# Optimization experiments

Hardware: AMD Instinct MI355X
Metric: run time of the kernel (lower is better)

The kernel has to match this reference:

```python
import jax, jax.numpy as jnp
import numpy as np

IN_FEATS, H_FEATS, OUT_FEATS = 128, 256, 64
N_NODES, N_EDGES = 50000, 800000
DROP_P = 0.5


def setup_inputs() -> dict:
    key = jax.random.key(0)
    k_h, k_e, k_w1, k_w2 = jax.random.split(key, 4)
    h = jax.random.normal(k_h, (N_NODES, IN_FEATS), dtype=jnp.float32)
    edge_index = jax.random.randint(k_e, (2, N_EDGES), 0, N_NODES, dtype=jnp.int64)
    # Glorot-style init for GraphConv weights; bias zeros (DGL default)
    W1 = jax.random.normal(k_w1, (IN_FEATS, H_FEATS), dtype=jnp.float32) / np.sqrt(IN_FEATS)
    b1 = jnp.zeros((H_FEATS,), dtype=jnp.float32)
    W2 = jax.random.normal(k_w2, (H_FEATS, OUT_FEATS), dtype=jnp.float32) / np.sqrt(H_FEATS)
    b2 = jnp.zeros((OUT_FEATS,), dtype=jnp.float32)
    return {"h": h, "W1": W1, "b1": b1, "W2": W2, "b2": b2,
            "edge_index": edge_index, "n_nodes": N_NODES}


def _sym_norm(edge_index, n_nodes):
    # symmetric GCN norm: deg^-1/2 on both endpoints (in-degree, clamped to 1)
    dst = edge_index[1]
    deg = jax.ops.segment_sum(jnp.ones(edge_index.shape[1], jnp.float32), dst,
                              num_segments=n_nodes)
    return jnp.where(deg > 0, deg, 1.0) ** -0.5  # [N]


def _graph_conv(h, W, b, src, dst, norm, n_nodes, apply_w_first):
    # DGL GraphConv (norm='both'): scale by src norm, aggregate, scale by dst norm.
    # W is applied before aggregation if in_feats > out_feats, else after.
    x = h * norm[:, None]
    if apply_w_first:
        x = x @ W
    agg = jax.ops.segment_sum(x[src], dst, num_segments=n_nodes)
    if not apply_w_first:
        agg = agg @ W
    return agg * norm[:, None] + b


def reference(h, W1, b1, W2, b2, edge_index, n_nodes):
    src, dst = edge_index[0], edge_index[1]
    norm = _sym_norm(edge_index, n_nodes)
    # layer 1: in(128) <= out(256) -> aggregate then transform; relu activation
    h1 = jax.nn.relu(_graph_conv(h, W1, b1, src, dst, norm, n_nodes, apply_w_first=False))
    # dropout(0.5), training mode, deterministic key
    keep = jax.random.bernoulli(jax.random.key(42), 1.0 - DROP_P, h1.shape)
    h1 = jnp.where(keep, h1 / (1.0 - DROP_P), 0.0)
    # layer 2: in(256) > out(64) -> transform then aggregate; no activation
    out = _graph_conv(h1, W2, b2, src, dst, norm, n_nodes, apply_w_first=True)
    return out
```

## Files before the change

kernel.cpp:

```cpp
#include <hip/hip_runtime.h>
#include <stdint.h>

#define N_IN  128
#define N_H   256
#define N_OUT 64
#define CHK   2048
#define CAP   6144

typedef __attribute__((ext_vector_type(8))) __bf16 bf16x8;
typedef __attribute__((ext_vector_type(4))) float f32x4;

__device__ __forceinline__ void tf4(uint32_t& x0, uint32_t& x1,
                                    const int r0, const int r1, const int r2, const int r3) {
  x0 += x1; x1 = (x1 << r0) | (x1 >> (32 - r0)); x1 ^= x0;
  x0 += x1; x1 = (x1 << r1) | (x1 >> (32 - r1)); x1 ^= x0;
  x0 += x1; x1 = (x1 << r2) | (x1 >> (32 - r2)); x1 ^= x0;
  x0 += x1; x1 = (x1 << r3) | (x1 >> (32 - r3)); x1 ^= x0;
}

__device__ __forceinline__ uint2 threefry2x32(uint32_t k0, uint32_t k1, uint32_t x0, uint32_t x1) {
  const uint32_t k2 = k0 ^ k1 ^ 0x1BD11BDAu;
  x0 += k0; x1 += k1;
  tf4(x0, x1, 13, 15, 26, 6);   x0 += k1; x1 += k2 + 1u;
  tf4(x0, x1, 17, 29, 16, 24);  x0 += k2; x1 += k0 + 2u;
  tf4(x0, x1, 13, 15, 26, 6);   x0 += k0; x1 += k1 + 3u;
  tf4(x0, x1, 17, 29, 16, 24);  x0 += k1; x1 += k2 + 4u;
  tf4(x0, x1, 13, 15, 26, 6);   x0 += k2; x1 += k0 + 5u;
  return make_uint2(x0, x1);
}

__device__ __forceinline__ uint16_t f2bf_rne(float v) {
  uint32_t b = __builtin_bit_cast(uint32_t, v);
  b += 0x7fffu + ((b >> 16) & 1u);
  return (uint16_t)(b >> 16);
}
__device__ __forceinline__ float bflo(uint32_t w) { return __builtin_bit_cast(float, w << 16); }
__device__ __forceinline__ float bfhi(uint32_t w) { return __builtin_bit_cast(float, w & 0xffff0000u); }

__device__ __forceinline__ void packW_body(const float* __restrict__ W,
                                           uint4* __restrict__ WH, uint4* __restrict__ WL,
                                           int Ncols, int nct, int nks, int g) {
  if (g >= nct * nks * 64) return;
  int lane = g & 63;
  int grp = g >> 6;
  int ks = grp % nks, ct = grp / nks;
  int k0 = ks * 32 + (lane >> 4) * 8;
  int col = ct * 16 + (lane & 15);
  uint32_t hb[8], lb[8];
#pragma unroll
  for (int j = 0; j < 8; j++) {
    float w = W[(size_t)(k0 + j) * Ncols + col];
    uint32_t bits = __builtin_bit_cast(uint32_t, w);
    uint32_t hi = bits & 0xffff0000u;
    float lo = w - __builtin_bit_cast(float, hi);
    hb[j] = hi >> 16;
    lb[j] = __builtin_bit_cast(uint32_t, lo) >> 16;
  }
  WH[g] = make_uint4(hb[0] | (hb[1] << 16), hb[2] | (hb[3] << 16),
                     hb[4] | (hb[5] << 16), hb[6] | (hb[7] << 16));
  WL[g] = make_uint4(lb[0] | (lb[1] << 16), lb[2] | (lb[3] << 16),
                     lb[4] | (lb[5] << 16), lb[6] | (lb[7] << 16));
}

__global__ __launch_bounds__(256) void k_front(
    const int* __restrict__ eidx, int E, int* __restrict__ bktCur, uint2* __restrict__ eb,
    uint16_t* __restrict__ mask, int N,
    const float* __restrict__ W1, uint4* __restrict__ W1H, uint4* __restrict__ W1L,
    const float* __restrict__ W2, uint4* __restrict__ W2H, uint4* __restrict__ W2L,
    int NBE) {
  const int b = blockIdx.x, t = threadIdx.x;
  if (b < NBE) {
    __shared__ int s_nz;
    __shared__ int hist[256];
    __shared__ int base[256];
    if (t == 0) s_nz = 0;
    hist[t] = 0;
    __syncthreads();
    int n = E < 2048 ? E : 2048;
    int nz = 0;
    for (int i = t; i < n; i += 256) nz |= (eidx[2 * i + 1] != 0) ? 1 : 0;
    if (nz) atomicAdd(&s_nz, 1);
    __syncthreads();
    int stride = (s_nz == 0) ? 2 : 1;

    int cb = b * CHK;
    int dc[8], sc[8];
#pragma unroll
    for (int i = 0; i < 8; i++) {
      int e = cb + i * 256 + t;
      if (e < E) {
        dc[i] = eidx[(size_t)(E + e) * stride];
        sc[i] = eidx[(size_t)e * stride];
        atomicAdd(&hist[dc[i] >> 8], 1);
      } else dc[i] = -1;
    }
    __syncthreads();
    int hcnt = hist[t];
    if (hcnt) base[t] = atomicAdd(&bktCur[t], hcnt);
    __syncthreads();
    hist[t] = 0;
    __syncthreads();
#pragma unroll
    for (int i = 0; i < 8; i++) {
      if (dc[i] >= 0) {
        int bk = dc[i] >> 8;
        int r = atomicAdd(&hist[bk], 1);
        eb[(size_t)bk * CAP + base[bk] + r] = make_uint2((unsigned)sc[i], (unsigned)dc[i]);
      }
    }
  } else {
    const int NBM = (N * 16 + 255) >> 8;
    int bb = b - NBE;
    if (bb < NBM) {
      int g = bb * 256 + t;
      if (g >= N * 16) return;
      uint32_t row = (uint32_t)(g >> 4), colb = (uint32_t)(g & 15);
      uint32_t bse = row * 256u + colb;
      uint32_t m = 0;
#pragma unroll
      for (int ct = 0; ct < 16; ct++) {
        uint2 o = threefry2x32(0u, 42u, 0u, bse + (uint32_t)ct * 16u);
        uint32_t bits = o.x ^ o.y;
        m |= ((~bits) >> 31) << ct;
      }
      mask[g] = (uint16_t)m;
    } else if (bb < NBM + 16) {
      packW_body(W1, W1H, W1L, N_H, 16, 4, (bb - NBM) * 256 + t);
    } else {
      packW_body(W2, W2H, W2L, N_OUT, 4, 8, (bb - NBM - 16) * 256 + t);
    }
  }
}

__global__ __launch_bounds__(256) void k_bucket_csr(
    const uint2* __restrict__ eb, const int* __restrict__ bktCur,
    int* __restrict__ rowptr, float* __restrict__ norm,
    int* __restrict__ esrc, int N, int E) {
  __shared__ int s[256];
  __shared__ int cnt[256];
  __shared__ int pfx[256];
  __shared__ int cur[256];
  const int b = blockIdx.x, t = threadIdx.x;
  if (b == 0 && t == 0) rowptr[N] = E;
  if (b * 256 >= N) return;
  int xc = bktCur[t];
  s[t] = xc;
  __syncthreads();
  for (int off = 1; off < 256; off <<= 1) {
    int u = (t >= off) ? s[t - off] : 0;
    __syncthreads();
    s[t] += u;
    __syncthreads();
  }
  const int lo = (b > 0) ? s[b - 1] : 0;
  const int ecnt = s[b] - lo;
  const uint2* ebb = eb + (size_t)b * CAP;
  cnt[t] = 0;
  __syncthreads();
  for (int e = t; e < ecnt; e += 256)
    atomicAdd(&cnt[ebb[e].y & 255u], 1);
  __syncthreads();
  int x = cnt[t];
  pfx[t] = x;
  __syncthreads();
  for (int off = 1; off < 256; off <<= 1) {
    int u = (t >= off) ? pfx[t - off] : 0;
    __syncthreads();
    pfx[t] += u;
    __syncthreads();
  }
  int excl = pfx[t] - x;
  int node = b * 256 + t;
  if (node < N) {
    rowptr[node] = lo + excl;
    norm[node] = x > 0 ? rsqrtf((float)x) : 1.0f;
  }
  cur[t] = excl;
  __syncthreads();
  for (int e = t; e < ecnt; e += 256) {
    uint2 r = ebb[e];
    int d = (int)(r.y & 255u);
    int p = atomicAdd(&cur[d], 1);
    esrc[lo + p] = (int)r.x;
  }
}

__global__ __launch_bounds__(256) void k_mid(
    int* __restrict__ esrc, const int* __restrict__ rowptr, int N,
    const float* __restrict__ h, const float* __restrict__ norm,
    uint16_t* __restrict__ hn, int NS) {
  const int b = blockIdx.x, t = threadIdx.x;
  if (b < NS) {
    int node = b * 4 + (t >> 6);
    if (node >= N) return;
    const int lane = t & 63;
    int lo = rowptr[node], hi = rowptr[node + 1], d = hi - lo;
    if (d <= 1) return;
    if (d <= 64) {
      int v = (lane < d) ? esrc[lo + lane] : 0x7fffffff;
#pragma unroll
      for (int k = 2; k <= 64; k <<= 1) {
#pragma unroll
        for (int j = k >> 1; j > 0; j >>= 1) {
          int other = __shfl_xor(v, j);
          bool up = ((lane & k) == 0);
          bool lower = ((lane & j) == 0);
          int mn = min(v, other), mx = max(v, other);
          v = (up == lower) ? mn : mx;
        }
      }
      if (lane < d) esrc[lo + lane] = v;
    } else if (lane == 0) {
      for (int i = lo + 1; i < hi; i++) {
        int v = esrc[i];
        int j = i - 1;
        while (j >= lo && esrc[j] > v) { esrc[j + 1] = esrc[j]; j--; }
        esrc[j + 1] = v;
      }
    }
  } else {
    int g = (b - NS) * 256 + t;
    if (g >= N * 32) return;
    float nr = norm[g >> 5];
    float4 v = *reinterpret_cast<const float4*>(h + (size_t)g * 4);
    ushort4 r;
    r.x = f2bf_rne(v.x * nr);
    r.y = f2bf_rne(v.y * nr);
    r.z = f2bf_rne(v.z * nr);
    r.w = f2bf_rne(v.w * nr);
    *reinterpret_cast<ushort4*>(hn + (size_t)g * 4) = r;
  }
}

__global__ __launch_bounds__(256) void k_pull1(
    const uint16_t* __restrict__ hn, const int* __restrict__ rowptr,
    const int* __restrict__ esrc, uint16_t* __restrict__ aggB, int N) {
  int node = blockIdx.x * 8 + (threadIdx.x >> 5);
  if (node >= N) return;
  int lane = threadIdx.x & 31;
  int lo = rowptr[node], hi = rowptr[node + 1];
  float4 a0 = {0,0,0,0}, a1 = {0,0,0,0}, a2 = {0,0,0,0}, a3 = {0,0,0,0};
  int e = lo;
  for (; e + 7 < hi; e += 8) {
    int s0 = esrc[e],     s1 = esrc[e + 1], s2 = esrc[e + 2], s3 = esrc[e + 3];
    int s4 = esrc[e + 4], s5 = esrc[e + 5], s6 = esrc[e + 6], s7 = esrc[e + 7];
    uint2 v0 = *reinterpret_cast<const uint2*>(hn + (size_t)s0 * N_IN + lane * 4);
    uint2 v1 = *reinterpret_cast<const uint2*>(hn + (size_t)s1 * N_IN + lane * 4);
    uint2 v2 = *reinterpret_cast<const uint2*>(hn + (size_t)s2 * N_IN + lane * 4);
    uint2 v3 = *reinterpret_cast<const uint2*>(hn + (size_t)s3 * N_IN + lane * 4);
    uint2 v4 = *reinterpret_cast<const uint2*>(hn + (size_t)s4 * N_IN + lane * 4);
    uint2 v5 = *reinterpret_cast<const uint2*>(hn + (size_t)s5 * N_IN + lane * 4);
    uint2 v6 = *reinterpret_cast<const uint2*>(hn + (size_t)s6 * N_IN + lane * 4);
    uint2 v7 = *reinterpret_cast<const uint2*>(hn + (size_t)s7 * N_IN + lane * 4);
    a0.x += bflo(v0.x); a0.y += bfhi(v0.x); a0.z += bflo(v0.y); a0.w += bfhi(v0.y);
    a1.x += bflo(v1.x); a1.y += bfhi(v1.x); a1.z += bflo(v1.y); a1.w += bfhi(v1.y);
    a2.x += bflo(v2.x); a2.y += bfhi(v2.x); a2.z += bflo(v2.y); a2.w += bfhi(v2.y);
    a3.x += bflo(v3.x); a3.y += bfhi(v3.x); a3.z += bflo(v3.y); a3.w += bfhi(v3.y);
    a0.x += bflo(v4.x); a0.y += bfhi(v4.x); a0.z += bflo(v4.y); a0.w += bfhi(v4.y);
    a1.x += bflo(v5.x); a1.y += bfhi(v5.x); a1.z += bflo(v5.y); a1.w += bfhi(v5.y);
    a2.x += bflo(v6.x); a2.y += bfhi(v6.x); a2.z += bflo(v6.y); a2.w += bfhi(v6.y);
    a3.x += bflo(v7.x); a3.y += bfhi(v7.x); a3.z += bflo(v7.y); a3.w += bfhi(v7.y);
  }
  for (; e < hi; e++) {
    uint2 v0 = *reinterpret_cast<const uint2*>(hn + (size_t)esrc[e] * N_IN + lane * 4);
    a0.x += bflo(v0.x); a0.y += bfhi(v0.x); a0.z += bflo(v0.y); a0.w += bfhi(v0.y);
  }
  float4 r;
  r.x = (a0.x + a1.x) + (a2.x + a3.x);
  r.y = (a0.y + a1.y) + (a2.y + a3.y);
  r.z = (a0.z + a1.z) + (a2.z + a3.z);
  r.w = (a0.w + a1.w) + (a2.w + a3.w);
  ushort4 p = make_ushort4(f2bf_rne(r.x), f2bf_rne(r.y), f2bf_rne(r.z), f2bf_rne(r.w));
  *reinterpret_cast<ushort4*>(aggB + (size_t)node * N_IN + lane * 4) = p;
}

__global__ __launch_bounds__(256) void k_gemm12(
    const uint16_t* __restrict__ aggB,
    const uint4* __restrict__ W1H, const uint4* __restrict__ W1L,
    const float* __restrict__ b1, const float* __restrict__ norm,
    const uint16_t* __restrict__ mask,
    const uint4* __restrict__ W2H, const uint4* __restrict__ W2L,
    uint16_t* __restrict__ zbf, int Nn) {
  __shared__ uint16_t h1[64 * 256];
  __shared__ uint4 wlds[2048];
  const int tid = threadIdx.x;
  const int wave = tid >> 6, lane = tid & 63;
  const int row0 = blockIdx.x * 64 + wave * 16;
  const int lrow = lane & 15, lk = lane >> 4;
  int arow = row0 + lrow; if (arow >= Nn) arow = Nn - 1;

  uint4 aq[4];
#pragma unroll
  for (int ks = 0; ks < 4; ks++)
    aq[ks] = *reinterpret_cast<const uint4*>(aggB + (size_t)arow * N_IN + ks * 32 + lk * 8);

  f32x4 acc[16];
#pragma unroll
  for (int c = 0; c < 16; c++) acc[c] = f32x4{0.f, 0.f, 0.f, 0.f};

  for (int ks = 0; ks < 4; ks++) {
    __syncthreads();
#pragma unroll
    for (int i = 0; i < 4; i++) {
      int g = tid + i * 256;
      int src = ((g >> 6) * 4 + ks) * 64 + (g & 63);
      wlds[g]        = W1H[src];
      wlds[1024 + g] = W1L[src];
    }
    __syncthreads();
    union { uint4 q; bf16x8 v; } ah; ah.q = aq[ks];
#pragma unroll
    for (int c = 0; c < 16; c++) {
      union { uint4 q; bf16x8 v; } bh, bl;
      bh.q = wlds[c * 64 + lane];
      bl.q = wlds[1024 + c * 64 + lane];
      acc[c] = __builtin_amdgcn_mfma_f32_16x16x32_bf16(ah.v, bh.v, acc[c], 0, 0, 0);
      acc[c] = __builtin_amdgcn_mfma_f32_16x16x32_bf16(ah.v, bl.v, acc[c], 0, 0, 0);
    }
  }

  const int colb = lane & 15, rgrp = lane >> 4;
#pragma unroll
  for (int r = 0; r < 4; r++) {
    int lrw = wave * 16 + rgrp * 4 + r;
    int row = blockIdx.x * 64 + lrw;
    float nr = (row < Nn) ? norm[row] : 0.f;
    uint32_t m = (row < Nn) ? (uint32_t)mask[row * 16 + colb] : 0u;
    int sw = (lrw & 7) << 3;
#pragma unroll
    for (int c = 0; c < 16; c++) {
      int col = c * 16 + colb;
      float v = fmaf(acc[c][r], nr, b1[col]);
      v = fmaxf(v, 0.f);
      v = ((m >> c) & 1u) ? v * (2.0f * nr) : 0.f;
      h1[lrw * 256 + (col ^ sw)] = f2bf_rne(v);
    }
  }

  f32x4 acc2[4];
#pragma unroll
  for (int c = 0; c < 4; c++) acc2[c] = f32x4{0.f, 0.f, 0.f, 0.f};
  const int myrow = wave * 16 + lrow;
  const int sw2 = (myrow & 7) << 3;

  for (int half = 0; half < 2; half++) {
    __syncthreads();
#pragma unroll
    for (int i = 0; i < 4; i++) {
      int g = tid + i * 256;
      int src = ((g >> 8) * 8 + half * 4 + ((g >> 6) & 3)) * 64 + (g & 63);
      wlds[g]        = W2H[src];
      wlds[1024 + g] = W2L[src];
    }
    __syncthreads();
#pragma unroll
    for (int ksl = 0; ksl < 4; ksl++) {
      int ks = half * 4 + ksl;
      union { uint4 q; bf16x8 v; } ah;
      int c0 = (ks * 32 + lk * 8) ^ sw2;
      ah.q = *reinterpret_cast<const uint4*>(&h1[myrow * 256 + c0]);
#pragma unroll
      for (int c = 0; c < 4; c++) {
        union { uint4 q; bf16x8 v; } bh, bl;
        bh.q = wlds[(c * 4 + ksl) * 64 + lane];
        bl.q = wlds[1024 + (c * 4 + ksl) * 64 + lane];
        acc2[c] = __builtin_amdgcn_mfma_f32_16x16x32_bf16(ah.v, bh.v, acc2[c], 0, 0, 0);
        acc2[c] = __builtin_amdgcn_mfma_f32_16x16x32_bf16(ah.v, bl.v, acc2[c], 0, 0, 0);
      }
    }
  }
#pragma unroll
  for (int r = 0; r < 4; r++) {
    int row = row0 + rgrp * 4 + r;
    if (row >= Nn) continue;
#pragma unroll
    for (int c = 0; c < 4; c++)
      zbf[(size_t)row * N_OUT + c * 16 + colb] = f2bf_rne(acc2[c][r]);
  }
}

__global__ __launch_bounds__(256) void k_pull2(
    const uint16_t* __restrict__ zbf, const float* __restrict__ norm,
    const float* __restrict__ b2, const int* __restrict__ rowptr,
    const int* __restrict__ esrc, float* __restrict__ out, int N) {
  int node = blockIdx.x * 16 + (threadIdx.x >> 4);
  if (node >= N) return;
  int lane = threadIdx.x & 15;
  int lo = rowptr[node], hi = rowptr[node + 1];
  float4 a0 = {0,0,0,0}, a1 = {0,0,0,0}, a2 = {0,0,0,0}, a3 = {0,0,0,0};
  int e = lo;
  for (; e + 7 < hi; e += 8) {
    int s0 = esrc[e],     s1 = esrc[e + 1], s2 = esrc[e + 2], s3 = esrc[e + 3];
    int s4 = esrc[e + 4], s5 = esrc[e + 5], s6 = esrc[e + 6], s7 = esrc[e + 7];
    uint2 v0 = *reinterpret_cast<const uint2*>(zbf + (size_t)s0 * N_OUT + lane * 4);
    uint2 v1 = *reinterpret_cast<const uint2*>(zbf + (size_t)s1 * N_OUT + lane * 4);
    uint2 v2 = *reinterpret_cast<const uint2*>(zbf + (size_t)s2 * N_OUT + lane * 4);
    uint2 v3 = *reinterpret_cast<const uint2*>(zbf + (size_t)s3 * N_OUT + lane * 4);
    uint2 v4 = *reinterpret_cast<const uint2*>(zbf + (size_t)s4 * N_OUT + lane * 4);
    uint2 v5 = *reinterpret_cast<const uint2*>(zbf + (size_t)s5 * N_OUT + lane * 4);
    uint2 v6 = *reinterpret_cast<const uint2*>(zbf + (size_t)s6 * N_OUT + lane * 4);
    uint2 v7 = *reinterpret_cast<const uint2*>(zbf + (size_t)s7 * N_OUT + lane * 4);
    a0.x += bflo(v0.x); a0.y += bfhi(v0.x); a0.z += bflo(v0.y); a0.w += bfhi(v0.y);
    a1.x += bflo(v1.x); a1.y += bfhi(v1.x); a1.z += bflo(v1.y); a1.w += bfhi(v1.y);
    a2.x += bflo(v2.x); a2.y += bfhi(v2.x); a2.z += bflo(v2.y); a2.w += bfhi(v2.y);
    a3.x += bflo(v3.x); a3.y += bfhi(v3.x); a3.z += bflo(v3.y); a3.w += bfhi(v3.y);
    a0.x += bflo(v4.x); a0.y += bfhi(v4.x); a0.z += bflo(v4.y); a0.w += bfhi(v4.y);
    a1.x += bflo(v5.x); a1.y += bfhi(v5.x); a1.z += bflo(v5.y); a1.w += bfhi(v5.y);
    a2.x += bflo(v6.x); a2.y += bfhi(v6.x); a2.z += bflo(v6.y); a2.w += bfhi(v6.y);
    a3.x += bflo(v7.x); a3.y += bfhi(v7.x); a3.z += bflo(v7.y); a3.w += bfhi(v7.y);
  }
  for (; e < hi; e++) {
    uint2 v0 = *reinterpret_cast<const uint2*>(zbf + (size_t)esrc[e] * N_OUT + lane * 4);
    a0.x += bflo(v0.x); a0.y += bfhi(v0.x); a0.z += bflo(v0.y); a0.w += bfhi(v0.y);
  }
  float nn = norm[node];
  float4 bb = *reinterpret_cast<const float4*>(b2 + lane * 4);
  float4 r;
  r.x = ((a0.x + a1.x) + (a2.x + a3.x)) * nn + bb.x;
  r.y = ((a0.y + a1.y) + (a2.y + a3.y)) * nn + bb.y;
  r.z = ((a0.z + a1.z) + (a2.z + a3.z)) * nn + bb.z;
  r.w = ((a0.w + a1.w) + (a2.w + a3.w)) * nn + bb.w;
  *reinterpret_cast<float4*>(out + (size_t)node * N_OUT + lane * 4) = r;
}

extern "C" void kernel_launch(void* const* d_in, const int* in_sizes, int n_in,
                              void* d_out, int out_size, void* d_ws, size_t ws_size,
                              hipStream_t stream) {
  const float* h  = (const float*)d_in[0];
  const float* W1 = (const float*)d_in[1];
  const float* b1 = (const float*)d_in[2];
  const float* W2 = (const float*)d_in[3];
  const float* b2 = (const float*)d_in[4];
  const int* eidx = (const int*)d_in[5];
  const int N = in_sizes[0] / N_IN;
  const int E = in_sizes[5] / 2;
  const int NBE = (E + CHK - 1) / CHK;
  const int NBM = (N * 16 + 255) / 256;
  const int NS  = (N + 3) / 4;
  const int NH  = (N * 32 + 255) / 256;

  char* ws = (char*)d_ws;
  size_t off = 0;
  auto alloc = [&](size_t bytes) { void* p = ws + off; off += (bytes + 511) & ~(size_t)511; return p; };
  int*      rowptr = (int*)alloc((size_t)(N + 1) * 4);
  float*    norm   = (float*)alloc((size_t)N * 4);
  int*      esrc   = (int*)alloc((size_t)E * 4);
  int*      bktCur = (int*)alloc((size_t)256 * 4);
  uint16_t* mask   = (uint16_t*)alloc((size_t)N * 16 * 2);
  uint4*    W1H    = (uint4*)alloc((size_t)16 * 4 * 64 * 16);
  uint4*    W1L    = (uint4*)alloc((size_t)16 * 4 * 64 * 16);
  uint4*    W2H    = (uint4*)alloc((size_t)4 * 8 * 64 * 16);
  uint4*    W2L    = (uint4*)alloc((size_t)4 * 8 * 64 * 16);
  uint2*    eb     = (uint2*)alloc((size_t)256 * CAP * 8);
  uint16_t* hn     = (uint16_t*)alloc((size_t)N * N_IN * 2);
  uint16_t* aggB   = (uint16_t*)alloc((size_t)N * N_IN * 2);
  uint16_t* zbf    = (uint16_t*)alloc((size_t)N * N_OUT * 2);
  float*    out    = (float*)d_out;

  hipMemsetAsync(bktCur, 0, 256 * 4, stream);

  k_front<<<NBE + NBM + 16 + 8, 256, 0, stream>>>(eidx, E, bktCur, eb,
                                                  mask, N, W1, W1H, W1L, W2, W2H, W2L, NBE);

  k_bucket_csr<<<256, 256, 0, stream>>>(eb, bktCur, rowptr, norm, esrc, N, E);

  k_mid<<<NS + NH, 256, 0, stream>>>(esrc, rowptr, N, h, norm, hn, NS);

  k_pull1<<<(N + 7) / 8, 256, 0, stream>>>(hn, rowptr, esrc, aggB, N);

  k_gemm12<<<(N + 63) / 64, 256, 0, stream>>>(aggB, W1H, W1L, b1, norm, mask,
                                              W2H, W2L, zbf, N);

  k_pull2<<<(N + 15) / 16, 256, 0, stream>>>(zbf, norm, b2, rowptr, esrc, out, N);
}
```

Measured before the change: 145.9 us.

## Fuse hn conversion into CSR build and sort neighbor lists inside pull kernels

After: 153.1 us. 5.0% more time.

```diff
diff --git a/kernel.cpp b/kernel.cpp
--- a/kernel.cpp
+++ b/kernel.cpp
@@ -36,6 +36,22 @@
 }
 __device__ __forceinline__ float bflo(uint32_t w) { return __builtin_bit_cast(float, w << 16); }
 __device__ __forceinline__ float bfhi(uint32_t w) { return __builtin_bit_cast(float, w & 0xffff0000u); }
+__device__ __forceinline__ float bfu16(uint16_t w) { return __builtin_bit_cast(float, (uint32_t)w << 16); }
+
+__device__ __forceinline__ int bitonic64(int v, int lane) {
+#pragma unroll
+  for (int k = 2; k <= 64; k <<= 1) {
+#pragma unroll
+    for (int j = k >> 1; j > 0; j >>= 1) {
+      int other = __shfl_xor(v, j);
+      bool up = ((lane & k) == 0);
+      bool lower = ((lane & j) == 0);
+      int mn = min(v, other), mx = max(v, other);
+      v = (up == lower) ? mn : mx;
+    }
+  }
+  return v;
+}
 
 __device__ __forceinline__ void packW_body(const float* __restrict__ W,
                                            uint4* __restrict__ WH, uint4* __restrict__ WL,
@@ -135,11 +151,13 @@
 __global__ __launch_bounds__(256) void k_bucket_csr(
     const uint2* __restrict__ eb, const int* __restrict__ bktCur,
     int* __restrict__ rowptr, float* __restrict__ norm,
-    int* __restrict__ esrc, int N, int E) {
+    int* __restrict__ esrc, const float* __restrict__ h,
+    uint16_t* __restrict__ hn, int N, int E) {
   __shared__ int s[256];
   __shared__ int cnt[256];
   __shared__ int pfx[256];
   __shared__ int cur[256];
+  __shared__ float narr[256];
   const int b = blockIdx.x, t = threadIdx.x;
   if (b == 0 && t == 0) rowptr[N] = E;
   if (b * 256 >= N) return;
@@ -171,9 +189,11 @@
   }
   int excl = pfx[t] - x;
   int node = b * 256 + t;
+  float nrm = x > 0 ? rsqrtf((float)x) : 1.0f;
+  narr[t] = nrm;
   if (node < N) {
     rowptr[node] = lo + excl;
-    norm[node] = x > 0 ? rsqrtf((float)x) : 1.0f;
+    norm[node] = nrm;
   }
   cur[t] = excl;
   __syncthreads();
@@ -183,34 +203,66 @@
     int p = atomicAdd(&cur[d], 1);
     esrc[lo + p] = (int)r.x;
   }
-}
-
-__global__ __launch_bounds__(256) void k_mid(
-    int* __restrict__ esrc, const int* __restrict__ rowptr, int N,
-    const float* __restrict__ h, const float* __restrict__ norm,
-    uint16_t* __restrict__ hn, int NS) {
-  const int b = blockIdx.x, t = threadIdx.x;
-  if (b < NS) {
-    int node = b * 4 + (t >> 6);
-    if (node >= N) return;
-    const int lane = t & 63;
-    int lo = rowptr[node], hi = rowptr[node + 1], d = hi - lo;
-    if (d <= 1) return;
-    if (d <= 64) {
-      int v = (lane < d) ? esrc[lo + lane] : 0x7fffffff;
-#pragma unroll
-      for (int k = 2; k <= 64; k <<= 1) {
-#pragma unroll
-        for (int j = k >> 1; j > 0; j >>= 1) {
-          int other = __shfl_xor(v, j);
-          bool up = ((lane & k) == 0);
-          bool lower = ((lane & j) == 0);
-          int mn = min(v, other), mx = max(v, other);
-          v = (up == lower) ? mn : mx;
-        }
-      }
-      if (lane < d) esrc[lo + lane] = v;
-    } else if (lane == 0) {
+  const int nrows = min(256, N - b * 256);
+#pragma unroll 4
+  for (int i = 0; i < 32; i++) {
+    int g = i * 256 + t;
+    int r = g >> 5;
+    if (r >= nrows) break;
+    int c4 = g & 31;
+    size_t row = (size_t)(b * 256 + r);
+    float4 v = *reinterpret_cast<const float4*>(h + row * N_IN + c4 * 4);
+    float nr = narr[r];
+    ushort4 o;
+    o.x = f2bf_rne(v.x * nr);
+    o.y = f2bf_rne(v.y * nr);
+    o.z = f2bf_rne(v.z * nr);
+    o.w = f2bf_rne(v.w * nr);
+    *reinterpret_cast<ushort4*>(hn + row * N_IN + c4 * 4) = o;
+  }
+}
+
+__global__ __launch_bounds__(256) void k_pull1s(
+    const uint16_t* __restrict__ hn, const int* __restrict__ rowptr,
+    int* esrc, uint16_t* __restrict__ aggB, int N) {
+  int node = blockIdx.x * 4 + (threadIdx.x >> 6);
+  if (node >= N) return;
+  const int lane = threadIdx.x & 63;
+  int lo = rowptr[node], hi = rowptr[node + 1], d = hi - lo;
+  float2 a0 = {0,0}, a1 = {0,0}, a2 = {0,0}, a3 = {0,0};
+  if (d <= 64) {
+    int v = (lane < d) ? esrc[lo + lane] : 0x7fffffff;
+    if (d > 1) v = bitonic64(v, lane);
+    int e = 0;
+    for (; e + 7 < d; e += 8) {
+      int s0 = __shfl(v, e),     s1 = __shfl(v, e + 1);
+      int s2 = __shfl(v, e + 2), s3 = __shfl(v, e + 3);
+      int s4 = __shfl(v, e + 4), s5 = __shfl(v, e + 5);
+      int s6 = __shfl(v, e + 6), s7 = __shfl(v, e + 7);
+      uint32_t u0 = *reinterpret_cast<const uint32_t*>(hn + (size_t)s0 * N_IN + lane * 2);
+      uint32_t u1 = *reinterpret_cast<const uint32_t*>(hn + (size_t)s1 * N_IN + lane * 2);
+      uint32_t u2 = *reinterpret_cast<const uint32_t*>(hn + (size_t)s2 * N_IN + lane * 2);
+      uint32_t u3 = *reinterpret_cast<const uint32_t*>(hn + (size_t)s3 * N_IN + lane * 2);
+      uint32_t u4 = *reinterpret_cast<const uint32_t*>(hn + (size_t)s4 * N_IN + lane * 2);
+      uint32_t u5 = *reinterpret_cast<const uint32_t*>(hn + (size_t)s5 * N_IN + lane * 2);
+      uint32_t u6 = *reinterpret_cast<const uint32_t*>(hn + (size_t)s6 * N_IN + lane * 2);
+      uint32_t u7 = *reinterpret_cast<const uint32_t*>(hn + (size_t)s7 * N_IN + lane * 2);
+      a0.x += bflo(u0); a0.y += bfhi(u0);
+      a1.x += bflo(u1); a1.y += bfhi(u1);
+      a2.x += bflo(u2); a2.y += bfhi(u2);
+      a3.x += bflo(u3); a3.y += bfhi(u3);
+      a0.x += bflo(u4); a0.y += bfhi(u4);
+      a1.x += bflo(u5); a1.y += bfhi(u5);
+      a2.x += bflo(u6); a2.y += bfhi(u6);
+      a3.x += bflo(u7); a3.y += bfhi(u7);
+    }
+    for (; e < d; e++) {
+      int s0 = __shfl(v, e);
+      uint32_t u0 = *reinterpret_cast<const uint32_t*>(hn + (size_t)s0 * N_IN + lane * 2);
+      a0.x += bflo(u0); a0.y += bfhi(u0);
+    }
+  } else {
+    if (lane == 0) {
       for (int i = lo + 1; i < hi; i++) {
         int v = esrc[i];
         int j = i - 1;
@@ -218,60 +270,17 @@
         esrc[j + 1] = v;
       }
     }
-  } else {
-    int g = (b - NS) * 256 + t;
-    if (g >= N * 32) return;
-    float nr = norm[g >> 5];
-    float4 v = *reinterpret_cast<const float4*>(h + (size_t)g * 4);
-    ushort4 r;
-    r.x = f2bf_rne(v.x * nr);
-    r.y = f2bf_rne(v.y * nr);
-    r.z = f2bf_rne(v.z * nr);
-    r.w = f2bf_rne(v.w * nr);
-    *reinterpret_cast<ushort4*>(hn + (size_t)g * 4) = r;
-  }
-}
-
-__global__ __launch_bounds__(256) void k_pull1(
-    const uint16_t* __restrict__ hn, const int* __restrict__ rowptr,
-    const int* __restrict__ esrc, uint16_t* __restrict__ aggB, int N) {
-  int node = blockIdx.x * 8 + (threadIdx.x >> 5);
-  if (node >= N) return;
-  int lane = threadIdx.x & 31;
-  int lo = rowptr[node], hi = rowptr[node + 1];
-  float4 a0 = {0,0,0,0}, a1 = {0,0,0,0}, a2 = {0,0,0,0}, a3 = {0,0,0,0};
-  int e = lo;
-  for (; e + 7 < hi; e += 8) {
-    int s0 = esrc[e],     s1 = esrc[e + 1], s2 = esrc[e + 2], s3 = esrc[e + 3];
-    int s4 = esrc[e + 4], s5 = esrc[e + 5], s6 = esrc[e + 6], s7 = esrc[e + 7];
-    uint2 v0 = *reinterpret_cast<const uint2*>(hn + (size_t)s0 * N_IN + lane * 4);
-    uint2 v1 = *reinterpret_cast<const uint2*>(hn + (size_t)s1 * N_IN + lane * 4);
-    uint2 v2 = *reinterpret_cast<const uint2*>(hn + (size_t)s2 * N_IN + lane * 4);
-    uint2 v3 = *reinterpret_cast<const uint2*>(hn + (size_t)s3 * N_IN + lane * 4);
-    uint2 v4 = *reinterpret_cast<const uint2*>(hn + (size_t)s4 * N_IN + lane * 4);
-    uint2 v5 = *reinterpret_cast<const uint2*>(hn + (size_t)s5 * N_IN + lane * 4);
-    uint2 v6 = *reinterpret_cast<const uint2*>(hn + (size_t)s6 * N_IN + lane * 4);
-    uint2 v7 = *reinterpret_cast<const uint2*>(hn + (size_t)s7 * N_IN + lane * 4);
-    a0.x += bflo(v0.x); a0.y += bfhi(v0.x); a0.z += bflo(v0.y); a0.w += bfhi(v0.y);
-    a1.x += bflo(v1.x); a1.y += bfhi(v1.x); a1.z += bflo(v1.y); a1.w += bfhi(v1.y);
-    a2.x += bflo(v2.x); a2.y += bfhi(v2.x); a2.z += bflo(v2.y); a2.w += bfhi(v2.y);
-    a3.x += bflo(v3.x); a3.y += bfhi(v3.x); a3.z += bflo(v3.y); a3.w += bfhi(v3.y);
-    a0.x += bflo(v4.x); a0.y += bfhi(v4.x); a0.z += bflo(v4.y); a0.w += bfhi(v4.y);
-    a1.x += bflo(v5.x); a1.y += bfhi(v5.x); a1.z += bflo(v5.y); a1.w += bfhi(v5.y);
-    a2.x += bflo(v6.x); a2.y += bfhi(v6.x); a2.z += bflo(v6.y); a2.w += bfhi(v6.y);
-    a3.x += bflo(v7.x); a3.y += bfhi(v7.x); a3.z += bflo(v7.y); a3.w += bfhi(v7.y);
-  }
-  for (; e < hi; e++) {
-    uint2 v0 = *reinterpret_cast<const uint2*>(hn + (size_t)esrc[e] * N_IN + lane * 4);
-    a0.x += bflo(v0.x); a0.y += bfhi(v0.x); a0.z += bflo(v0.y); a0.w += bfhi(v0.y);
-  }
-  float4 r;
+    for (int e = 0; e < d; e++) {
+      int s0 = esrc[lo + e];
+      uint32_t u0 = *reinterpret_cast<const uint32_t*>(hn + (size_t)s0 * N_IN + lane * 2);
+      a0.x += bflo(u0); a0.y += bfhi(u0);
+    }
+  }
+  float2 r;
   r.x = (a0.x + a1.x) + (a2.x + a3.x);
   r.y = (a0.y + a1.y) + (a2.y + a3.y);
-  r.z = (a0.z + a1.z) + (a2.z + a3.z);
-  r.w = (a0.w + a1.w) + (a2.w + a3.w);
-  ushort4 p = make_ushort4(f2bf_rne(r.x), f2bf_rne(r.y), f2bf_rne(r.z), f2bf_rne(r.w));
-  *reinterpret_cast<ushort4*>(aggB + (size_t)node * N_IN + lane * 4) = p;
+  ushort2 p = make_ushort2(f2bf_rne(r.x), f2bf_rne(r.y));
+  *reinterpret_cast<ushort2*>(aggB + (size_t)node * N_IN + lane * 2) = p;
 }
 
 __global__ __launch_bounds__(256) void k_gemm12(
@@ -379,48 +388,55 @@
   }
 }
 
-__global__ __launch_bounds__(256) void k_pull2(
+__global__ __launch_bounds__(256) void k_pull2s(
     const uint16_t* __restrict__ zbf, const float* __restrict__ norm,
     const float* __restrict__ b2, const int* __restrict__ rowptr,
-    const int* __restrict__ esrc, float* __restrict__ out, int N) {
-  int node = blockIdx.x * 16 + (threadIdx.x >> 4);
+    int* esrc, float* __restrict__ out, int N) {
+  int node = blockIdx.x * 4 + (threadIdx.x >> 6);
   if (node >= N) return;
-  int lane = threadIdx.x & 15;
-  int lo = rowptr[node], hi = rowptr[node + 1];
-  float4 a0 = {0,0,0,0}, a1 = {0,0,0,0}, a2 = {0,0,0,0}, a3 = {0,0,0,0};
-  int e = lo;
-  for (; e + 7 < hi; e += 8) {
-    int s0 = esrc[e],     s1 = esrc[e + 1], s2 = esrc[e + 2], s3 = esrc[e + 3];
-    int s4 = esrc[e + 4], s5 = esrc[e + 5], s6 = esrc[e + 6], s7 = esrc[e + 7];
-    uint2 v0 = *reinterpret_cast<const uint2*>(zbf + (size_t)s0 * N_OUT + lane * 4);
-    uint2 v1 = *reinterpret_cast<const uint2*>(zbf + (size_t)s1 * N_OUT + lane * 4);
-    uint2 v2 = *reinterpret_cast<const uint2*>(zbf + (size_t)s2 * N_OUT + lane * 4);
-    uint2 v3 = *reinterpret_cast<const uint2*>(zbf + (size_t)s3 * N_OUT + lane * 4);
-    uint2 v4 = *reinterpret_cast<const uint2*>(zbf + (size_t)s4 * N_OUT + lane * 4);
-    uint2 v5 = *reinterpret_cast<const uint2*>(zbf + (size_t)s5 * N_OUT + lane * 4);
-    uint2 v6 = *reinterpret_cast<const uint2*>(zbf + (size_t)s6 * N_OUT + lane * 4);
-    uint2 v7 = *reinterpret_cast<const uint2*>(zbf + (size_t)s7 * N_OUT + lane * 4);
-    a0.x += bflo(v0.x); a0.y += bfhi(v0.x); a0.z += bflo(v0.y); a0.w += bfhi(v0.y);
-    a1.x += bflo(v1.x); a1.y += bfhi(v1.x); a1.z += bflo(v1.y); a1.w += bfhi(v1.y);
-    a2.x += bflo(v2.x); a2.y += bfhi(v2.x); a2.z += bflo(v2.y); a2.w += bfhi(v2.y);
-    a3.x += bflo(v3.x); a3.y += bfhi(v3.x); a3.z += bflo(v3.y); a3.w += bfhi(v3.y);
-    a0.x += bflo(v4.x); a0.y += bfhi(v4.x); a0.z += bflo(v4.y); a0.w += bfhi(v4.y);
-    a1.x += bflo(v5.x); a1.y += bfhi(v5.x); a1.z += bflo(v5.y); a1.w += bfhi(v5.y);
-    a2.x += bflo(v6.x); a2.y += bfhi(v6.x); a2.z += bflo(v6.y); a2.w += bfhi(v6.y);
-    a3.x += bflo(v7.x); a3.y += bfhi(v7.x); a3.z += bflo(v7.y); a3.w += bfhi(v7.y);
-  }
-  for (; e < hi; e++) {
-    uint2 v0 = *reinterpret_cast<const uint2*>(zbf + (size_t)esrc[e] * N_OUT + lane * 4);
-    a0.x += bflo(v0.x); a0.y += bfhi(v0.x); a0.z += bflo(v0.y); a0.w += bfhi(v0.y);
-  }
-  float nn = norm[node];
-  float4 bb = *reinterpret_cast<const float4*>(b2 + lane * 4);
-  float4 r;
-  r.x = ((a0.x + a1.x) + (a2.x + a3.x)) * nn + bb.x;
-  r.y = ((a0.y + a1.y) + (a2.y + a3.y)) * nn + bb.y;
-  r.z = ((a0.z + a1.z) + (a2.z + a3.z)) * nn + bb.z;
-  r.w = ((a0.w + a1.w) + (a2.w + a3.w)) * nn + bb.w;
-  *reinterpret_cast<float4*>(out + (size_t)node * N_OUT + lane * 4) = r;
+  const int lane = threadIdx.x & 63;
+  int lo = rowptr[node], hi = rowptr[node + 1], d = hi - lo;
+  float a0 = 0.f, a1 = 0.f, a2 = 0.f, a3 = 0.f;
+  if (d <= 64) {
+    int v = (lane < d) ? esrc[lo + lane] : 0x7fffffff;
+    if (d > 1) v = bitonic64(v, lane);
+    int e = 0;
+    for (; e + 7 < d; e += 8) {
+      int s0 = __shfl(v, e),     s1 = __shfl(v, e + 1);
+      int s2 = __shfl(v, e + 2), s3 = __shfl(v, e + 3);
+      int s4 = __shfl(v, e + 4), s5 = __shfl(v, e + 5);
+      int s6 = __shfl(v, e + 6), s7 = __shfl(v, e + 7);
+      uint16_t u0 = zbf[(size_t)s0 * N_OUT + lane];
+      uint16_t u1 = zbf[(size_t)s1 * N_OUT + lane];
+      uint16_t u2 = zbf[(size_t)s2 * N_OUT + lane];
+      uint16_t u3 = zbf[(size_t)s3 * N_OUT + lane];
+      uint16_t u4 = zbf[(size_t)s4 * N_OUT + lane];
+      uint16_t u5 = zbf[(size_t)s5 * N_OUT + lane];
+      uint16_t u6 = zbf[(size_t)s6 * N_OUT + lane];
+      uint16_t u7 = zbf[(size_t)s7 * N_OUT + lane];
+      a0 += bfu16(u0); a1 += bfu16(u1); a2 += bfu16(u2); a3 += bfu16(u3);
+      a0 += bfu16(u4); a1 += bfu16(u5); a2 += bfu16(u6); a3 += bfu16(u7);
+    }
+    for (; e < d; e++) {
+      int s0 = __shfl(v, e);
+      a0 += bfu16(zbf[(size_t)s0 * N_OUT + lane]);
+    }
+  } else {
+    if (lane == 0) {
+      for (int i = lo + 1; i < hi; i++) {
+        int v = esrc[i];
+        int j = i - 1;
+        while (j >= lo && esrc[j] > v) { esrc[j + 1] = esrc[j]; j--; }
+        esrc[j + 1] = v;
+      }
+    }
+    for (int e = 0; e < d; e++) {
+      int s0 = esrc[lo + e];
+      a0 += bfu16(zbf[(size_t)s0 * N_OUT + lane]);
+    }
+  }
+  float r = ((a0 + a1) + (a2 + a3)) * norm[node] + b2[lane];
+  out[(size_t)node * N_OUT + lane] = r;
 }
 
 extern "C" void kernel_launch(void* const* d_in, const int* in_sizes, int n_in,
@@ -436,8 +452,6 @@
   const int E = in_sizes[5] / 2;
   const int NBE = (E + CHK - 1) / CHK;
   const int NBM = (N * 16 + 255) / 256;
-  const int NS  = (N + 3) / 4;
-  const int NH  = (N * 32 + 255) / 256;
 
   char* ws = (char*)d_ws;
   size_t off = 0;
@@ -462,14 +476,12 @@
   k_front<<<NBE + NBM + 16 + 8, 256, 0, stream>>>(eidx, E, bktCur, eb,
                                                   mask, N, W1, W1H, W1L, W2, W2H, W2L, NBE);
 
-  k_bucket_csr<<<256, 256, 0, stream>>>(eb, bktCur, rowptr, norm, esrc, N, E);
-
-  k_mid<<<NS + NH, 256, 0, stream>>>(esrc, rowptr, N, h, norm, hn, NS);
-
-  k_pull1<<<(N + 7) / 8, 256, 0, stream>>>(hn, rowptr, esrc, aggB, N);
+  k_bucket_csr<<<256, 256, 0, stream>>>(eb, bktCur, rowptr, norm, esrc, h, hn, N, E);
+
+  k_pull1s<<<(N + 3) / 4, 256, 0, stream>>>(hn, rowptr, esrc, aggB, N);
 
   k_gemm12<<<(N + 63) / 64, 256, 0, stream>>>(aggB, W1H, W1L, b1, norm, mask,
                                               W2H, W2L, zbf, N);
 
-  k_pull2<<<(N + 15) / 16, 256, 0, stream>>>(zbf, norm, b2, rowptr, esrc, out, N);
-}
+  k_pull2s<<<(N + 3) / 4, 256, 0, stream>>>(zbf, norm, b2, rowptr, esrc, out, N);
+}
```
